# Performance work log

Hardware: AMD Instinct MI355X
Metric: run time of the kernel (lower is better)

## Reference

```python
import jax, jax.numpy as jnp
import numpy as np

D_MODEL = 256
N_HEADS = 8
HEAD_DIM = D_MODEL // N_HEADS


def setup_inputs() -> dict:
    key = jax.random.key(0)
    k1, k2, k3, k4, k5, k6, k7 = jax.random.split(key, 7)
    B, T, N, D = 4, 32, 32, D_MODEL
    x = jax.random.normal(k1, (B, T, N, D), dtype=jnp.float32)
    bias_features = jax.random.normal(k2, (B, T, N, N, D), dtype=jnp.float32)
    # alive mask, mostly True so rows are rarely fully masked
    mask = jax.random.uniform(k3, (B, T, N)) < 0.9
    s = 1.0 / np.sqrt(D)
    w_qkv = jax.random.normal(k4, (D, 3 * D), dtype=jnp.float32) * s
    b_qkv = jnp.zeros((3 * D,), dtype=jnp.float32)
    w_proj = jax.random.normal(k5, (D, D), dtype=jnp.float32) * s
    b_proj = jnp.zeros((D,), dtype=jnp.float32)
    return {"x": x, "bias_features": bias_features, "mask": mask,
            "w_qkv": w_qkv, "b_qkv": b_qkv, "w_proj": w_proj, "b_proj": b_proj}


def reference(x, bias_features, mask, w_qkv, b_qkv, w_proj, b_proj):
    B, T, N, D = x.shape
    H, Dh = N_HEADS, D // N_HEADS
    Bt = B * T
    xf = x.reshape(Bt, N, D)
    qkv = xf @ w_qkv + b_qkv                       # (Bt, N, 3D)
    q, k, v = jnp.split(qkv, 3, axis=-1)
    q = q.reshape(Bt, N, H, Dh)
    k = k.reshape(Bt, N, H, Dh)
    v = v.reshape(Bt, N, H, Dh)
    b_geo = bias_features.reshape(Bt, N, N, H, Dh)
    k_pair = k[:, None] + b_geo                    # (Bt, N, N, H, Dh)
    v_pair = v[:, None] + b_geo
    # scores: (Bt, H, N, N)
    scores = jnp.einsum('bihd,bijhd->bhij', q, k_pair) * (Dh ** -0.5)
    mask_flat = mask.reshape(Bt, 1, 1, N)
    scores = jnp.where(mask_flat, scores, -jnp.inf)
    max_scores = jnp.max(scores, axis=-1, keepdims=True)
    is_nan_row = max_scores == -jnp.inf
    scores_safe = jnp.where(is_nan_row, 0.0, scores)
    attn = jax.nn.softmax(scores_safe, axis=-1)
    attn = jnp.where(is_nan_row, 0.0, attn)
    out = jnp.einsum('bhij,bijhd->bihd', attn, v_pair).reshape(Bt, N, D)
    out = out.reshape(B, T, N, D)
    return out @ w_proj + b_proj
```

## Files before the change

kernel.cpp:

```cpp
#include <hip/hip_runtime.h>
#include <math.h>

typedef __attribute__((ext_vector_type(8))) short bf16x8;
typedef __attribute__((ext_vector_type(4))) short bf16x4;
typedef __attribute__((ext_vector_type(4))) float f32x4;

__device__ inline ushort f2bf(float f) {
    union { float f; uint u; } v; v.f = f;
    uint u = v.u;
    return (ushort)((u + 0x7fff + ((u >> 16) & 1)) >> 16);
}
__device__ inline float bf2f(ushort u) {
    union { uint u; float f; } v; v.u = ((uint)u) << 16; return v.f;
}

template<int BM, int BN, int WGM, int WGN, int MODE>
__global__ __launch_bounds__(WGM * WGN * 64) void gemm_fused(
    const void* __restrict__ Ap, const float* __restrict__ Bw, int ldb,
    const float* __restrict__ bias,
    void* __restrict__ C0, void* __restrict__ C1, void* __restrict__ C2,
    int K, int N)
{
    constexpr int BK = 32;
    constexpr int NT = WGM * WGN * 64;
    constexpr int WM = BM / (WGM * 16);
    constexpr int WN = BN / (WGN * 16);

    __shared__ ushort As[BM * BK];
    __shared__ ushort Bs[BN * BK];

    const int tid = threadIdx.x;
    const int lane = tid & 63, wid = tid >> 6;
    const int wm = wid / WGN, wn = wid % WGN;
    const int row0 = blockIdx.y * BM, col0 = blockIdx.x * BN;
    const int frow = lane & 15, fg = lane >> 4;

    f32x4 acc[WM][WN] = {};

    for (int k0 = 0; k0 < K; k0 += BK) {
        if constexpr (MODE == 0) {
            #pragma unroll
            for (int ci = tid; ci < BM * 8; ci += NT) {
                int r = ci >> 3, kq = ci & 7, g = kq >> 1;
                float4 v = *(const float4*)((const float*)Ap + (size_t)(row0 + r) * K + k0 + kq * 4);
                bf16x4 o;
                o[0] = (short)f2bf(v.x); o[1] = (short)f2bf(v.y);
                o[2] = (short)f2bf(v.z); o[3] = (short)f2bf(v.w);
                *(bf16x4*)&As[r * 32 + ((g ^ ((r >> 1) & 3)) << 3) + (kq & 1) * 4] = o;
            }
        } else {
            #pragma unroll
            for (int ci = tid; ci < BM * 4; ci += NT) {
                int r = ci >> 2, g = ci & 3;
                bf16x8 v = *(const bf16x8*)((const ushort*)Ap + (size_t)(row0 + r) * K + k0 + g * 8);
                *(bf16x8*)&As[r * 32 + ((g ^ ((r >> 1) & 3)) << 3)] = v;
            }
        }
        #pragma unroll
        for (int ci = tid; ci < BN * 8; ci += NT) {
            int kk = ci & 31, n4 = ci >> 5;
            float4 v = *(const float4*)&Bw[(size_t)(k0 + kk) * ldb + col0 + n4 * 4];
            float vv[4] = {v.x, v.y, v.z, v.w};
            #pragma unroll
            for (int e = 0; e < 4; ++e) {
                int n = n4 * 4 + e;
                Bs[n * 32 + (((kk >> 3) ^ ((n >> 1) & 3)) << 3) + (kk & 7)] = f2bf(vv[e]);
            }
        }
        __syncthreads();

        bf16x8 af[WM], bfr[WN];
        #pragma unroll
        for (int m = 0; m < WM; ++m) {
            int r = (wm * WM + m) * 16 + frow;
            af[m] = *(const bf16x8*)&As[r * 32 + ((fg ^ ((r >> 1) & 3)) << 3)];
        }
        #pragma unroll
        for (int n = 0; n < WN; ++n) {
            int r = (wn * WN + n) * 16 + frow;
            bfr[n] = *(const bf16x8*)&Bs[r * 32 + ((fg ^ ((r >> 1) & 3)) << 3)];
        }
        #pragma unroll
        for (int m = 0; m < WM; ++m)
            #pragma unroll
            for (int n = 0; n < WN; ++n)
                acc[m][n] = __builtin_amdgcn_mfma_f32_16x16x32_bf16(
                    af[m], bfr[n], acc[m][n], 0, 0, 0);
        __syncthreads();
    }

    #pragma unroll
    for (int n = 0; n < WN; ++n) {
        int gcol = col0 + (wn * WN + n) * 16 + frow;
        float bv = bias[gcol];
        if constexpr (MODE == 0) {
            int b = gcol >> 8, c = gcol & 255;
            ushort* dst = (b == 0) ? (ushort*)C0 : (b == 1) ? (ushort*)C1 : (ushort*)C2;
            #pragma unroll
            for (int m = 0; m < WM; ++m) {
                int grow0 = row0 + (wm * WM + m) * 16 + fg * 4;
                #pragma unroll
                for (int r = 0; r < 4; ++r)
                    dst[(size_t)(grow0 + r) * 256 + c] = f2bf(acc[m][n][r] + bv);
            }
        } else {
            float* dst = (float*)C0;
            #pragma unroll
            for (int m = 0; m < WM; ++m) {
                int grow0 = row0 + (wm * WM + m) * 16 + fg * 4;
                #pragma unroll
                for (int r = 0; r < 4; ++r)
                    dst[(size_t)(grow0 + r) * N + gcol] = acc[m][n][r] + bv;
            }
        }
    }
}

__global__ __launch_bounds__(256) void relattn_kernel(
    const ushort* __restrict__ qb, const ushort* __restrict__ kb,
    const ushort* __restrict__ vb, const float* __restrict__ bias,
    const int* __restrict__ mask, ushort* __restrict__ attn_out)
{
    __shared__ ushort slab[4][32 * 64];

    const int blk = blockIdx.x;
    const int bt = blk >> 5;
    const int tid = threadIdx.x;
    const int w = tid >> 6, L = tid & 63;
    const int hw = L >> 5;
    const int h = 2 * w + hw;
    const int jd = L & 31;

    ushort* sl = slab[w];

    const float* bs = bias + (size_t)blk * 8192 + w * 64 + L;
    #pragma unroll
    for (int g = 0; g < 4; ++g) {
        float t0 = bs[(size_t)(g * 8 + 0) * 256];
        float t1 = bs[(size_t)(g * 8 + 1) * 256];
        float t2 = bs[(size_t)(g * 8 + 2) * 256];
        float t3 = bs[(size_t)(g * 8 + 3) * 256];
        float t4 = bs[(size_t)(g * 8 + 4) * 256];
        float t5 = bs[(size_t)(g * 8 + 5) * 256];
        float t6 = bs[(size_t)(g * 8 + 6) * 256];
        float t7 = bs[(size_t)(g * 8 + 7) * 256];
        float tt[8] = {t0, t1, t2, t3, t4, t5, t6, t7};
        #pragma unroll
        for (int r = 0; r < 8; ++r) {
            int j = g * 8 + r;
            sl[j * 64 + ((((L >> 3) ^ (j & 7)) << 3) | (L & 7))] = f2bf(tt[r]);
        }
    }

    const ushort* qrow = qb + (size_t)blk * 256 + h * 32;
    const ushort* krow = kb + (size_t)(bt * 32 + jd) * 256 + h * 32;
    float s = 0.f;
    #pragma unroll
    for (int t = 0; t < 4; ++t) {
        bf16x8 q8 = *(const bf16x8*)(qrow + t * 8);
        bf16x8 k8 = *(const bf16x8*)(krow + t * 8);
        int cc = hw * 4 + t;
        bf16x8 b8 = *(const bf16x8*)&sl[jd * 64 + ((cc ^ (jd & 7)) << 3)];
        #pragma unroll
        for (int e = 0; e < 8; ++e)
            s += bf2f((ushort)q8[e]) * (bf2f((ushort)k8[e]) + bf2f((ushort)b8[e]));
    }
    s *= 0.17677669529663687f;

    const bool alive = (mask[bt * 32 + jd] != 0);
    s = alive ? s : -__builtin_inff();

    float m = s;
    #pragma unroll
    for (int off = 16; off; off >>= 1) m = fmaxf(m, __shfl_xor(m, off));
    const bool dead = (m == -__builtin_inff());
    float p = alive ? __expf(s - m) : 0.f;
    float l = p;
    #pragma unroll
    for (int off = 16; off; off >>= 1) l += __shfl_xor(l, off);
    float pn = dead ? 0.f : p / l;

    const ushort* vcol = vb + (size_t)bt * 8192 + w * 64 + L;
    const int half = L & 32;
    float o0 = 0.f, o1 = 0.f, o2 = 0.f, o3 = 0.f;
    #pragma unroll
    for (int jq = 0; jq < 8; ++jq) {
        int j0 = jq * 4;
        float pa = __shfl(pn, half | (j0 + 0));
        float pb = __shfl(pn, half | (j0 + 1));
        float pc = __shfl(pn, half | (j0 + 2));
        float pd = __shfl(pn, half | (j0 + 3));
        float va = bf2f(vcol[(size_t)(j0 + 0) * 256]);
        float vbv = bf2f(vcol[(size_t)(j0 + 1) * 256]);
        float vc = bf2f(vcol[(size_t)(j0 + 2) * 256]);
        float vd = bf2f(vcol[(size_t)(j0 + 3) * 256]);
        float ba = bf2f(sl[(j0 + 0) * 64 + ((((L >> 3) ^ ((j0 + 0) & 7)) << 3) | (L & 7))]);
        float bb = bf2f(sl[(j0 + 1) * 64 + ((((L >> 3) ^ ((j0 + 1) & 7)) << 3) | (L & 7))]);
        float bc = bf2f(sl[(j0 + 2) * 64 + ((((L >> 3) ^ ((j0 + 2) & 7)) << 3) | (L & 7))]);
        float bd = bf2f(sl[(j0 + 3) * 64 + ((((L >> 3) ^ ((j0 + 3) & 7)) << 3) | (L & 7))]);
        o0 += pa * (va + ba);
        o1 += pb * (vbv + bb);
        o2 += pc * (vc + bc);
        o3 += pd * (vd + bd);
    }
    attn_out[(size_t)blk * 256 + w * 64 + L] = f2bf((o0 + o1) + (o2 + o3));
}

extern "C" void kernel_launch(void* const* d_in, const int* in_sizes, int n_in,
                              void* d_out, int out_size, void* d_ws, size_t ws_size,
                              hipStream_t stream) {
    const float* x      = (const float*)d_in[0];
    const float* bias_f = (const float*)d_in[1];
    const int*   mask   = (const int*)d_in[2];
    const float* w_qkv  = (const float*)d_in[3];
    const float* b_qkv  = (const float*)d_in[4];
    const float* w_proj = (const float*)d_in[5];
    const float* b_proj = (const float*)d_in[6];
    float* out = (float*)d_out;

    ushort* qb = (ushort*)d_ws;
    ushort* kb = qb + (size_t)4096 * 256;
    ushort* vb = kb + (size_t)4096 * 256;
    ushort* ao = vb + (size_t)4096 * 256;

    gemm_fused<64, 64, 2, 2, 0><<<dim3(12, 64), 256, 0, stream>>>(
        x, w_qkv, 768, b_qkv, qb, kb, vb, 256, 768);

    relattn_kernel<<<4096, 256, 0, stream>>>(qb, kb, vb, bias_f, mask, ao);

    gemm_fused<32, 64, 1, 4, 1><<<dim3(4, 128), 256, 0, stream>>>(
        ao, w_proj, 256, b_proj, out, nullptr, nullptr, 256, 256);
}
```

Before: 57.99 us.

## Process four query rows per block with register-prefetched bias slabs

The attention kernel now has each block handle four consecutive query rows of the same batch-time slice, and the grid shrinks by four. K rows and the mask are loaded once per block and reused. The next row's bias features are prefetched into registers as float4 vectors while the current row is computed, then converted and written to the per-wave LDS slab. This aims to hide the latency of the dominant bias stream and cut per-block launch overhead, at the cost of more registers per thread and fewer blocks in flight.

```diff
diff --git a/kernel.cpp b/kernel.cpp
--- a/kernel.cpp
+++ b/kernel.cpp
@@ -116,15 +116,16 @@
     }
 }
 
-__global__ __launch_bounds__(256) void relattn_kernel(
+__global__ __launch_bounds__(256, 4) void relattn_kernel(
     const ushort* __restrict__ qb, const ushort* __restrict__ kb,
     const ushort* __restrict__ vb, const float* __restrict__ bias,
     const int* __restrict__ mask, ushort* __restrict__ attn_out)
 {
     __shared__ ushort slab[4][32 * 64];
 
-    const int blk = blockIdx.x;
-    const int bt = blk >> 5;
+    const int b = blockIdx.x;
+    const int item0 = b << 2;
+    const int bt = item0 >> 5;
     const int tid = threadIdx.x;
     const int w = tid >> 6, L = tid & 63;
     const int hw = L >> 5;
@@ -132,78 +133,97 @@
     const int jd = L & 31;
 
     ushort* sl = slab[w];
-
-    const float* bs = bias + (size_t)blk * 8192 + w * 64 + L;
+    const int srow = L >> 4;
+    const int sc4 = L & 15;
+
+    const bool alive = (mask[bt * 32 + jd] != 0);
+
+    const ushort* krow = kb + (size_t)(bt * 32 + jd) * 256 + h * 32;
+    bf16x8 k8[4];
     #pragma unroll
-    for (int g = 0; g < 4; ++g) {
-        float t0 = bs[(size_t)(g * 8 + 0) * 256];
-        float t1 = bs[(size_t)(g * 8 + 1) * 256];
-        float t2 = bs[(size_t)(g * 8 + 2) * 256];
-        float t3 = bs[(size_t)(g * 8 + 3) * 256];
-        float t4 = bs[(size_t)(g * 8 + 4) * 256];
-        float t5 = bs[(size_t)(g * 8 + 5) * 256];
-        float t6 = bs[(size_t)(g * 8 + 6) * 256];
-        float t7 = bs[(size_t)(g * 8 + 7) * 256];
-        float tt[8] = {t0, t1, t2, t3, t4, t5, t6, t7};
-        #pragma unroll
-        for (int r = 0; r < 8; ++r) {
-            int j = g * 8 + r;
-            sl[j * 64 + ((((L >> 3) ^ (j & 7)) << 3) | (L & 7))] = f2bf(tt[r]);
-        }
+    for (int t = 0; t < 4; ++t) k8[t] = *(const bf16x8*)(krow + t * 8);
+
+    const ushort* vcol = vb + (size_t)bt * 8192 + w * 64 + L;
+    const float* bbase = bias + (size_t)item0 * 8192 + w * 64;
+
+    float4 pref[8];
+    #pragma unroll
+    for (int g = 0; g < 8; ++g)
+        pref[g] = *(const float4*)(bbase + (size_t)(g * 4 + srow) * 256 + sc4 * 4);
+
+    auto write_slab = [&]() {
+        #pragma unroll
+        for (int g = 0; g < 8; ++g) {
+            int j = g * 4 + srow;
+            int cc = sc4 >> 1, half = sc4 & 1;
+            bf16x4 o;
+            o[0] = (short)f2bf(pref[g].x); o[1] = (short)f2bf(pref[g].y);
+            o[2] = (short)f2bf(pref[g].z); o[3] = (short)f2bf(pref[g].w);
+            *(bf16x4*)&sl[j * 64 + ((cc ^ (j & 7)) << 3) + half * 4] = o;
+        }
+    };
+    write_slab();
+
+    for (int it = 0; it < 4; ++it) {
+        const int blk = item0 + it;
+
+        if (it < 3) {
+            const float* nb = bbase + (size_t)(it + 1) * 8192;
+            #pragma unroll
+            for (int g = 0; g < 8; ++g)
+                pref[g] = *(const float4*)(nb + (size_t)(g * 4 + srow) * 256 + sc4 * 4);
+        }
+
+        const ushort* qrow = qb + (size_t)blk * 256 + h * 32;
+        float s = 0.f;
+        #pragma unroll
+        for (int t = 0; t < 4; ++t) {
+            bf16x8 q8 = *(const bf16x8*)(qrow + t * 8);
+            int cc = hw * 4 + t;
+            bf16x8 b8 = *(const bf16x8*)&sl[jd * 64 + ((cc ^ (jd & 7)) << 3)];
+            #pragma unroll
+            for (int e = 0; e < 8; ++e)
+                s += bf2f((ushort)q8[e]) * (bf2f((ushort)k8[t][e]) + bf2f((ushort)b8[e]));
+        }
+        s *= 0.17677669529663687f;
+        s = alive ? s : -__builtin_inff();
+
+        float m = s;
+        #pragma unroll
+        for (int off = 16; off; off >>= 1) m = fmaxf(m, __shfl_xor(m, off));
+        const bool dead = (m == -__builtin_inff());
+        float p = alive ? __expf(s - m) : 0.f;
+        float l = p;
+        #pragma unroll
+        for (int off = 16; off; off >>= 1) l += __shfl_xor(l, off);
+        float pn = dead ? 0.f : p / l;
+
+        const int half32 = L & 32;
+        float o0 = 0.f, o1 = 0.f, o2 = 0.f, o3 = 0.f;
+        #pragma unroll
+        for (int jq = 0; jq < 8; ++jq) {
+            int j0 = jq * 4;
+            float pa = __shfl(pn, half32 | (j0 + 0));
+            float pb = __shfl(pn, half32 | (j0 + 1));
+            float pc = __shfl(pn, half32 | (j0 + 2));
+            float pd = __shfl(pn, half32 | (j0 + 3));
+            float va = bf2f(vcol[(size_t)(j0 + 0) * 256]);
+            float vbv = bf2f(vcol[(size_t)(j0 + 1) * 256]);
+            float vc = bf2f(vcol[(size_t)(j0 + 2) * 256]);
+            float vd = bf2f(vcol[(size_t)(j0 + 3) * 256]);
+            float ba = bf2f(sl[(j0 + 0) * 64 + ((((L >> 3) ^ ((j0 + 0) & 7)) << 3) | (L & 7))]);
+            float bb = bf2f(sl[(j0 + 1) * 64 + ((((L >> 3) ^ ((j0 + 1) & 7)) << 3) | (L & 7))]);
+            float bc = bf2f(sl[(j0 + 2) * 64 + ((((L >> 3) ^ ((j0 + 2) & 7)) << 3) | (L & 7))]);
+            float bd = bf2f(sl[(j0 + 3) * 64 + ((((L >> 3) ^ ((j0 + 3) & 7)) << 3) | (L & 7))]);
+            o0 += pa * (va + ba);
+            o1 += pb * (vbv + bb);
+            o2 += pc * (vc + bc);
+            o3 += pd * (vd + bd);
+        }
+        attn_out[(size_t)blk * 256 + w * 64 + L] = f2bf((o0 + o1) + (o2 + o3));
+
+        if (it < 3) write_slab();
     }
-
-    const ushort* qrow = qb + (size_t)blk * 256 + h * 32;
-    const ushort* krow = kb + (size_t)(bt * 32 + jd) * 256 + h * 32;
-    float s = 0.f;
-    #pragma unroll
-    for (int t = 0; t < 4; ++t) {
-        bf16x8 q8 = *(const bf16x8*)(qrow + t * 8);
-        bf16x8 k8 = *(const bf16x8*)(krow + t * 8);
-        int cc = hw * 4 + t;
-        bf16x8 b8 = *(const bf16x8*)&sl[jd * 64 + ((cc ^ (jd & 7)) << 3)];
-        #pragma unroll
-        for (int e = 0; e < 8; ++e)
-            s += bf2f((ushort)q8[e]) * (bf2f((ushort)k8[e]) + bf2f((ushort)b8[e]));
-    }
-    s *= 0.17677669529663687f;
-
-    const bool alive = (mask[bt * 32 + jd] != 0);
-    s = alive ? s : -__builtin_inff();
-
-    float m = s;
-    #pragma unroll
-    for (int off = 16; off; off >>= 1) m = fmaxf(m, __shfl_xor(m, off));
-    const bool dead = (m == -__builtin_inff());
-    float p = alive ? __expf(s - m) : 0.f;
-    float l = p;
-    #pragma unroll
-    for (int off = 16; off; off >>= 1) l += __shfl_xor(l, off);
-    float pn = dead ? 0.f : p / l;
-
-    const ushort* vcol = vb + (size_t)bt * 8192 + w * 64 + L;
-    const int half = L & 32;
-    float o0 = 0.f, o1 = 0.f, o2 = 0.f, o3 = 0.f;
-    #pragma unroll
-    for (int jq = 0; jq < 8; ++jq) {
-        int j0 = jq * 4;
-        float pa = __shfl(pn, half | (j0 + 0));
-        float pb = __shfl(pn, half | (j0 + 1));
-        float pc = __shfl(pn, half | (j0 + 2));
-        float pd = __shfl(pn, half | (j0 + 3));
-        float va = bf2f(vcol[(size_t)(j0 + 0) * 256]);
-        float vbv = bf2f(vcol[(size_t)(j0 + 1) * 256]);
-        float vc = bf2f(vcol[(size_t)(j0 + 2) * 256]);
-        float vd = bf2f(vcol[(size_t)(j0 + 3) * 256]);
-        float ba = bf2f(sl[(j0 + 0) * 64 + ((((L >> 3) ^ ((j0 + 0) & 7)) << 3) | (L & 7))]);
-        float bb = bf2f(sl[(j0 + 1) * 64 + ((((L >> 3) ^ ((j0 + 1) & 7)) << 3) | (L & 7))]);
-        float bc = bf2f(sl[(j0 + 2) * 64 + ((((L >> 3) ^ ((j0 + 2) & 7)) << 3) | (L & 7))]);
-        float bd = bf2f(sl[(j0 + 3) * 64 + ((((L >> 3) ^ ((j0 + 3) & 7)) << 3) | (L & 7))]);
-        o0 += pa * (va + ba);
-        o1 += pb * (vbv + bb);
-        o2 += pc * (vc + bc);
-        o3 += pd * (vd + bd);
-    }
-    attn_out[(size_t)blk * 256 + w * 64 + L] = f2bf((o0 + o1) + (o2 + o3));
 }
 
 extern "C" void kernel_launch(void* const* d_in, const int* in_sizes, int n_in,
@@ -226,7 +246,7 @@
     gemm_fused<64, 64, 2, 2, 0><<<dim3(12, 64), 256, 0, stream>>>(
         x, w_qkv, 768, b_qkv, qb, kb, vb, 256, 768);
 
-    relattn_kernel<<<4096, 256, 0, stream>>>(qb, kb, vb, bias_f, mask, ao);
+    relattn_kernel<<<1024, 256, 0, stream>>>(qb, kb, vb, bias_f, mask, ao);
 
     gemm_fused<32, 64, 1, 4, 1><<<dim3(4, 128), 256, 0, stream>>>(
         ao, w_proj, 256, b_proj, out, nullptr, nullptr, 256, 256);
```

Measured after the change: 97.26 us. 67.7% more time.
